# Kernel tuning notes

Measured on AMD Instinct MI355X. Metric: run time of the kernel, lower is better.

Reference implementation:

```python
import jax, jax.numpy as jnp
import numpy as np

MUL = 512
IR_DIMS = (1, 3, 5)          # 0e, 1e, 2e -> 2l+1
PW = MUL ** -0.5             # path_weight = (mul_in * n_paths_to_out)^-0.5, n_paths=1 each


def setup_inputs() -> dict:
    key = jax.random.key(0)
    k_x, k0, k1, k2 = jax.random.split(key, 4)
    B = 4096
    D = MUL * sum(IR_DIMS)  # 4608
    return {
        "x": jax.random.normal(k_x, (B, D), dtype=jnp.float32),
        "w0": jax.random.normal(k0, (MUL, MUL), dtype=jnp.float32),
        "w1": jax.random.normal(k1, (MUL, MUL), dtype=jnp.float32),
        "w2": jax.random.normal(k2, (MUL, MUL), dtype=jnp.float32),
        "b0": jnp.zeros((MUL,), dtype=jnp.float32),  # bias only on scalar 0e irrep
    }


def reference(x, w0, w1, w2, b0):
    B = x.shape[0]
    # split x into per-irrep blocks (B, mul, 2l+1), as Irreps.as_list does
    offs = np.cumsum([0] + [MUL * d for d in IR_DIMS])
    blocks = [x[:, offs[i]:offs[i + 1]].reshape(B, MUL, IR_DIMS[i]) for i in range(3)]
    outs = []
    for blk, w, d in zip(blocks, (w0, w1, w2), IR_DIMS):
        # path_weight * einsum('uw,bui->bwi'), then flatten to mul_ir_out.dim
        o = PW * jnp.einsum('uw,bui->bwi', w, blk)
        outs.append(o.reshape(B, MUL * d))
    # bias instruction: path_weight 1.0, only on the scalar (0e) output irrep
    outs[0] = outs[0] + b0[None, :]
    return jnp.concatenate(outs, axis=-1)
```

## Files before the change

kernel.cpp:

```cpp
#include <hip/hip_runtime.h>


#define BATCH 4096
#define DTOT 4608
#define NMUL 512

typedef __attribute__((ext_vector_type(8))) short short8;
typedef __attribute__((ext_vector_type(8))) unsigned short ushort8;
typedef __attribute__((ext_vector_type(4))) float float4v;

#define XPL_BYTES (9ull * BATCH * NMUL * 2)

__device__ __forceinline__ unsigned short f2bf(float f) {
    unsigned int u = __builtin_bit_cast(unsigned int, f);
    return (unsigned short)((u + 0x7fffu + ((u >> 16) & 1u)) >> 16);
}
__device__ __forceinline__ void gld16(const unsigned short* g, unsigned short* l) {
    __builtin_amdgcn_global_load_lds(
        (const __attribute__((address_space(1))) unsigned int*)(const void*)g,
        (__attribute__((address_space(3))) unsigned int*)(void*)l, 16, 0, 0);
}
__device__ __forceinline__ void colmap(int col, int& c, int& u) {
    if (col < 512)       { c = 0; u = col; }
    else if (col < 2048) { int t = col - 512;  c = 1 + t % 3; u = t / 3; }
    else                 { int t = col - 2048; c = 4 + t % 5; u = t / 5; }
}

__global__ __launch_bounds__(256) void prep(const float* __restrict__ x,
                                            const float* __restrict__ w0,
                                            const float* __restrict__ w1,
                                            const float* __restrict__ w2,
                                            unsigned short* __restrict__ Xp,
                                            unsigned short* __restrict__ Wt) {
    __shared__ unsigned short buf[4608];
    const int tid = threadIdx.x;
    const int b = blockIdx.x;
    if (b < BATCH) {
        const int row = b;
        const float4v* src = (const float4v*)(x + (size_t)row * DTOT);
        for (int p = tid; p < DTOT / 4; p += 256) {
            float4v v = src[p];
#pragma unroll
            for (int j = 0; j < 4; ++j) {
                int c, u; colmap(p * 4 + j, c, u);
                buf[c * NMUL + u] = f2bf(v[j]);
            }
        }
        __syncthreads();
        for (int q = tid; q < DTOT / 8; q += 256) {
            const int c = q >> 6, u8 = q & 63;
            *(ushort8*)(Xp + ((size_t)(c * BATCH + row) * NMUL) + u8 * 8) =
                *(const ushort8*)&buf[c * NMUL + u8 * 8];
        }
    } else {
        const int t = b - BATCH;
        const int ch = t >> 6, tt = t & 63;
        const int tk = (tt >> 3) * 64, tn = (tt & 7) * 64;
        const float* W = (ch == 0) ? w0 : (ch == 1) ? w1 : w2;
        const int r0 = tid >> 4, c4 = (tid & 15) * 4;
#pragma unroll
        for (int rr = 0; rr < 4; ++rr) {
            const int row = r0 + rr * 16;
            float4v v = *(const float4v*)(W + (size_t)(tk + row) * NMUL + tn + c4);
#pragma unroll
            for (int j = 0; j < 4; ++j) buf[(c4 + j) * 72 + row] = f2bf(v[j]);
        }
        __syncthreads();
        for (int q = tid; q < 512; q += 256) {
            const int nn = q >> 3, k8 = q & 7;
            *(ushort8*)(Wt + ((size_t)(ch * NMUL + tn + nn) * NMUL) + tk + k8 * 8) =
                *(const ushort8*)&buf[nn * 72 + k8 * 8];
        }
    }
}

template <int D, int PBASE, int XOFF, int WCH>
__device__ __forceinline__ void body_d35(int rel,
                                         const unsigned short* __restrict__ Xp,
                                         const unsigned short* __restrict__ Wt,
                                         float* __restrict__ out,
                                         unsigned short* As, unsigned short* Bs) {
    float* Cs = (float*)As;

    const int tid = threadIdx.x;
    const int lane = tid & 63;
    const int w = tid >> 6;
    const int lr = lane & 15;
    const int lq = lane >> 4;

    const int n0 = (rel & 7) * 64;
    const int m0 = (rel >> 3) * 64;

    const unsigned short* Ag =
        Xp + ((size_t)(PBASE + w) * BATCH + m0 + (lane >> 2)) * NMUL + (lane & 3) * 8;
    const unsigned short* Bg =
        Wt + ((size_t)WCH * NMUL + n0 + (lane >> 2)) * NMUL + (lane & 3) * 8;
    unsigned short* Al = As + w * 2048;

    float4v acc[4][4];
#pragma unroll
    for (int a = 0; a < 4; ++a)
#pragma unroll
        for (int b = 0; b < 4; ++b) acc[a][b] = (float4v)0.f;

    for (int kt = 0; kt < 16; ++kt) {
        const int ko = kt * 32;
        if (w < D) {
#pragma unroll
            for (int p = 0; p < 4; ++p)
                gld16(Ag + (size_t)p * 16 * NMUL + ko, Al + p * 512);
            for (int p = w; p < 4; p += D)
                gld16(Bg + (size_t)p * 16 * NMUL + ko, Bs + p * 512);
        }
        __syncthreads();
        if (w < D) {
            short8 af[4], bf[4];
#pragma unroll
            for (int mi = 0; mi < 4; ++mi)
                af[mi] = *(const short8*)(Al + (mi * 16 + lr) * 32 + lq * 8);
#pragma unroll
            for (int ni = 0; ni < 4; ++ni)
                bf[ni] = *(const short8*)(Bs + (ni * 16 + lr) * 32 + lq * 8);
#pragma unroll
            for (int mi = 0; mi < 4; ++mi)
#pragma unroll
                for (int ni = 0; ni < 4; ++ni)
                    acc[mi][ni] = __builtin_amdgcn_mfma_f32_16x16x32_bf16(
                        af[mi], bf[ni], acc[mi][ni], 0, 0, 0);
        }
        __syncthreads();
    }

    const float PW = 0.044194173824159216f;
#pragma unroll
    for (int mc = 0; mc < 4; ++mc) {
        if (w < D) {
#pragma unroll
            for (int ni = 0; ni < 4; ++ni)
#pragma unroll
                for (int r = 0; r < 4; ++r)
                    Cs[(lq * 4 + r) * (64 * D) + (ni * 16 + lr) * D + w] =
                        acc[mc][ni][r] * PW;
        }
        __syncthreads();
        constexpr int F4 = 16 * 16 * D;
        for (int f = tid; f < F4; f += 320) {
            const int row = f / (16 * D);
            const int c4  = f % (16 * D);
            *(float4v*)(out + (size_t)(m0 + mc * 16 + row) * DTOT + XOFF + n0 * D + c4 * 4) =
                *(const float4v*)(Cs + f * 4);
        }
        __syncthreads();
    }
}

__device__ __forceinline__ void body_d1(int rel,
                                        const unsigned short* __restrict__ Xp,
                                        const unsigned short* __restrict__ Wt,
                                        const float* __restrict__ b0,
                                        float* __restrict__ out,
                                        unsigned short* As, unsigned short* Bs) {
    const int tid = threadIdx.x;
    const int lane = tid & 63;
    const int w = tid >> 6;
    const int lr = lane & 15;
    const int lq = lane >> 4;
    const int wm = (w >> 1) * 64;
    const int wn = (w & 1) * 64;

    const int n0 = (rel & 3) * 128;
    const int m0 = (rel >> 2) * 128;

    const unsigned short* Ag = Xp + (size_t)(m0 + w * 32 + (lane >> 2)) * NMUL + (lane & 3) * 8;
    const unsigned short* Bg = Wt + (size_t)(n0 + w * 32 + (lane >> 2)) * NMUL + (lane & 3) * 8;
    unsigned short* Al = As + w * 1024;
    unsigned short* Bl = Bs + w * 1024;

    float4v acc[4][4];
#pragma unroll
    for (int a = 0; a < 4; ++a)
#pragma unroll
        for (int b = 0; b < 4; ++b) acc[a][b] = (float4v)0.f;

    for (int kt = 0; kt < 16; ++kt) {
        const int ko = kt * 32;
        if (w < 4) {
            gld16(Ag + ko, Al);
            gld16(Ag + ko + 16 * NMUL, Al + 512);
            gld16(Bg + ko, Bl);
            gld16(Bg + ko + 16 * NMUL, Bl + 512);
        }
        __syncthreads();
        if (w < 4) {
            short8 af[4], bf[4];
#pragma unroll
            for (int mi = 0; mi < 4; ++mi)
                af[mi] = *(const short8*)(As + (wm + mi * 16 + lr) * 32 + lq * 8);
#pragma unroll
            for (int ni = 0; ni < 4; ++ni)
                bf[ni] = *(const short8*)(Bs + (wn + ni * 16 + lr) * 32 + lq * 8);
#pragma unroll
            for (int mi = 0; mi < 4; ++mi)
#pragma unroll
                for (int ni = 0; ni < 4; ++ni)
                    acc[mi][ni] = __builtin_amdgcn_mfma_f32_16x16x32_bf16(
                        af[mi], bf[ni], acc[mi][ni], 0, 0, 0);
        }
        __syncthreads();
    }

    if (w < 4) {
        const float PW = 0.044194173824159216f;
#pragma unroll
        for (int ni = 0; ni < 4; ++ni) {
            const int col = n0 + wn + ni * 16 + lr;
            const float bias = b0[col];
#pragma unroll
            for (int mi = 0; mi < 4; ++mi)
#pragma unroll
                for (int r = 0; r < 4; ++r)
                    out[(size_t)(m0 + wm + mi * 16 + lq * 4 + r) * DTOT + col] =
                        acc[mi][ni][r] * PW + bias;
        }
    }
}

__global__ __launch_bounds__(320) void gemm_all(const unsigned short* __restrict__ Xp,
                                                const unsigned short* __restrict__ Wt,
                                                const float* __restrict__ b0,
                                                float* __restrict__ out) {
    __shared__ __align__(16) unsigned short As[10240];
    __shared__ __align__(16) unsigned short Bs[4096];

    const int b = blockIdx.x;
    if (b < 512)       body_d35<5, 4, 2048, 2>(b, Xp, Wt, out, As, Bs);
    else if (b < 1024) body_d35<3, 1, 512, 1>(b - 512, Xp, Wt, out, As, Bs);
    else               body_d1(b - 1024, Xp, Wt, b0, out, As, Bs);
}

extern "C" void kernel_launch(void* const* d_in, const int* in_sizes, int n_in,
                              void* d_out, int out_size, void* d_ws, size_t ws_size,
                              hipStream_t stream) {
    const float* x  = (const float*)d_in[0];
    const float* w0 = (const float*)d_in[1];
    const float* w1 = (const float*)d_in[2];
    const float* w2 = (const float*)d_in[3];
    const float* b0 = (const float*)d_in[4];
    float* out = (float*)d_out;

    unsigned short* Xp = (unsigned short*)d_ws;
    unsigned short* Wt = (unsigned short*)((char*)d_ws + XPL_BYTES);

    prep<<<dim3(BATCH + 192), dim3(256), 0, stream>>>(x, w0, w1, w2, Xp, Wt);
    gemm_all<<<dim3(1152), dim3(320), 0, stream>>>(Xp, Wt, b0, out);
}
```

Measured before the change: 192.9 us.

## Double-buffer LDS tiles, XOR-swizzle LDS layout, and remap blocks across XCDs

Both GEMM bodies now double-buffer their LDS tiles: the next K-slice is prefetched with global_load_lds while MFMAs run on the current one, which drops one barrier per iteration. Tile columns are XOR-swizzled on load and on read to avoid LDS bank conflicts. Block IDs are remapped so consecutive logical tiles land on the same XCD, improving L2 reuse. LDS use roughly doubles, which can lower occupancy.

```diff
diff --git a/kernel.cpp b/kernel.cpp
--- a/kernel.cpp
+++ b/kernel.cpp
@@ -79,9 +79,8 @@
                                          const unsigned short* __restrict__ Xp,
                                          const unsigned short* __restrict__ Wt,
                                          float* __restrict__ out,
-                                         unsigned short* As, unsigned short* Bs) {
-    float* Cs = (float*)As;
-
+                                         unsigned short (*As)[10240],
+                                         unsigned short (*Bs)[2048]) {
     const int tid = threadIdx.x;
     const int lane = tid & 63;
     const int w = tid >> 6;
@@ -91,11 +90,13 @@
     const int n0 = (rel & 7) * 64;
     const int m0 = (rel >> 3) * 64;
 
+    const int ksw = ((lane & 3) ^ ((lane >> 3) & 3)) * 8;
+    const int rsw = (lq ^ ((lr >> 1) & 3)) * 8;
+
     const unsigned short* Ag =
-        Xp + ((size_t)(PBASE + w) * BATCH + m0 + (lane >> 2)) * NMUL + (lane & 3) * 8;
+        Xp + ((size_t)(PBASE + w) * BATCH + m0 + (lane >> 2)) * NMUL + ksw;
     const unsigned short* Bg =
-        Wt + ((size_t)WCH * NMUL + n0 + (lane >> 2)) * NMUL + (lane & 3) * 8;
-    unsigned short* Al = As + w * 2048;
+        Wt + ((size_t)WCH * NMUL + n0 + (lane >> 2)) * NMUL + ksw;
 
     float4v acc[4][4];
 #pragma unroll
@@ -103,24 +104,37 @@
 #pragma unroll
         for (int b = 0; b < 4; ++b) acc[a][b] = (float4v)0.f;
 
+    if (w < D) {
+#pragma unroll
+        for (int p = 0; p < 4; ++p)
+            gld16(Ag + (size_t)p * 16 * NMUL, As[0] + w * 2048 + p * 512);
+    }
+    if (w < 4) gld16(Bg + (size_t)w * 16 * NMUL, Bs[0] + w * 512);
+    __syncthreads();
+
     for (int kt = 0; kt < 16; ++kt) {
-        const int ko = kt * 32;
+        const int cur = kt & 1;
+        if (kt < 15) {
+            const int ko = (kt + 1) * 32;
+            if (w < D) {
+#pragma unroll
+                for (int p = 0; p < 4; ++p)
+                    gld16(Ag + (size_t)p * 16 * NMUL + ko,
+                          As[cur ^ 1] + w * 2048 + p * 512);
+            }
+            if (w < 4)
+                gld16(Bg + (size_t)w * 16 * NMUL + ko, Bs[cur ^ 1] + w * 512);
+        }
         if (w < D) {
-#pragma unroll
-            for (int p = 0; p < 4; ++p)
-                gld16(Ag + (size_t)p * 16 * NMUL + ko, Al + p * 512);
-            for (int p = w; p < 4; p += D)
-                gld16(Bg + (size_t)p * 16 * NMUL + ko, Bs + p * 512);
-        }
-        __syncthreads();
-        if (w < D) {
+            const unsigned short* Al = As[cur] + w * 2048;
+            const unsigned short* Bl = Bs[cur];
             short8 af[4], bf[4];
 #pragma unroll
             for (int mi = 0; mi < 4; ++mi)
-                af[mi] = *(const short8*)(Al + (mi * 16 + lr) * 32 + lq * 8);
+                af[mi] = *(const short8*)(Al + (mi * 16 + lr) * 32 + rsw);
 #pragma unroll
             for (int ni = 0; ni < 4; ++ni)
-                bf[ni] = *(const short8*)(Bs + (ni * 16 + lr) * 32 + lq * 8);
+                bf[ni] = *(const short8*)(Bl + (ni * 16 + lr) * 32 + rsw);
 #pragma unroll
             for (int mi = 0; mi < 4; ++mi)
 #pragma unroll
@@ -131,6 +145,7 @@
         __syncthreads();
     }
 
+    float* Cs = (float*)As;
     const float PW = 0.044194173824159216f;
 #pragma unroll
     for (int mc = 0; mc < 4; ++mc) {
@@ -159,7 +174,7 @@
                                         const unsigned short* __restrict__ Wt,
                                         const float* __restrict__ b0,
                                         float* __restrict__ out,
-                                        unsigned short* As, unsigned short* Bs) {
+                                        unsigned short (*As)[10240]) {
     const int tid = threadIdx.x;
     const int lane = tid & 63;
     const int w = tid >> 6;
@@ -171,10 +186,11 @@
     const int n0 = (rel & 3) * 128;
     const int m0 = (rel >> 2) * 128;
 
-    const unsigned short* Ag = Xp + (size_t)(m0 + w * 32 + (lane >> 2)) * NMUL + (lane & 3) * 8;
-    const unsigned short* Bg = Wt + (size_t)(n0 + w * 32 + (lane >> 2)) * NMUL + (lane & 3) * 8;
-    unsigned short* Al = As + w * 1024;
-    unsigned short* Bl = Bs + w * 1024;
+    const int ksw = ((lane & 3) ^ ((lane >> 3) & 3)) * 8;
+    const int rsw = (lq ^ ((lr >> 1) & 3)) * 8;
+
+    const unsigned short* Ag = Xp + (size_t)(m0 + w * 32 + (lane >> 2)) * NMUL + ksw;
+    const unsigned short* Bg = Wt + (size_t)(n0 + w * 32 + (lane >> 2)) * NMUL + ksw;
 
     float4v acc[4][4];
 #pragma unroll
@@ -182,23 +198,33 @@
 #pragma unroll
         for (int b = 0; b < 4; ++b) acc[a][b] = (float4v)0.f;
 
+    if (w < 4) {
+        gld16(Ag, As[0] + w * 1024);
+        gld16(Ag + 16 * NMUL, As[0] + w * 1024 + 512);
+        gld16(Bg, As[0] + 4096 + w * 1024);
+        gld16(Bg + 16 * NMUL, As[0] + 4096 + w * 1024 + 512);
+    }
+    __syncthreads();
+
     for (int kt = 0; kt < 16; ++kt) {
-        const int ko = kt * 32;
+        const int cur = kt & 1;
+        if (kt < 15 && w < 4) {
+            const int ko = (kt + 1) * 32;
+            gld16(Ag + ko, As[cur ^ 1] + w * 1024);
+            gld16(Ag + ko + 16 * NMUL, As[cur ^ 1] + w * 1024 + 512);
+            gld16(Bg + ko, As[cur ^ 1] + 4096 + w * 1024);
+            gld16(Bg + ko + 16 * NMUL, As[cur ^ 1] + 4096 + w * 1024 + 512);
+        }
         if (w < 4) {
-            gld16(Ag + ko, Al);
-            gld16(Ag + ko + 16 * NMUL, Al + 512);
-            gld16(Bg + ko, Bl);
-            gld16(Bg + ko + 16 * NMUL, Bl + 512);
-        }
-        __syncthreads();
-        if (w < 4) {
+            const unsigned short* Ab = As[cur];
+            const unsigned short* Bb = As[cur] + 4096;
             short8 af[4], bf[4];
 #pragma unroll
             for (int mi = 0; mi < 4; ++mi)
-                af[mi] = *(const short8*)(As + (wm + mi * 16 + lr) * 32 + lq * 8);
+                af[mi] = *(const short8*)(Ab + (wm + mi * 16 + lr) * 32 + rsw);
 #pragma unroll
             for (int ni = 0; ni < 4; ++ni)
-                bf[ni] = *(const short8*)(Bs + (wn + ni * 16 + lr) * 32 + lq * 8);
+                bf[ni] = *(const short8*)(Bb + (wn + ni * 16 + lr) * 32 + rsw);
 #pragma unroll
             for (int mi = 0; mi < 4; ++mi)
 #pragma unroll
@@ -229,13 +255,16 @@
                                                 const unsigned short* __restrict__ Wt,
                                                 const float* __restrict__ b0,
                                                 float* __restrict__ out) {
-    __shared__ __align__(16) unsigned short As[10240];
-    __shared__ __align__(16) unsigned short Bs[4096];
-
-    const int b = blockIdx.x;
+    __shared__ __align__(16) unsigned short As[2][10240];
+    __shared__ __align__(16) unsigned short Bs[2][2048];
+
+    const int hw = blockIdx.x;
+    const int xcd = hw & 7, j = hw >> 3;
+    const int b = ((xcd + ((j >> 3) << 3)) << 3) + (j & 7);
+
     if (b < 512)       body_d35<5, 4, 2048, 2>(b, Xp, Wt, out, As, Bs);
     else if (b < 1024) body_d35<3, 1, 512, 1>(b - 512, Xp, Wt, out, As, Bs);
-    else               body_d1(b - 1024, Xp, Wt, b0, out, As, Bs);
+    else               body_d1(b - 1024, Xp, Wt, b0, out, As);
 }
 
 extern "C" void kernel_launch(void* const* d_in, const int* in_sizes, int n_in,
```

Result: faster. 177.3 us (-8.1%).

## Swizzle LDS tiles, remap blocks across XCDs, and lighten GEMM barriers

Applied to the files above, without the earlier changes.

Applies an XOR swizzle to the k-chunk offsets in both the global-to-LDS loads and the LDS fragment reads to reduce bank conflicts. Remaps block indices so neighbouring output tiles land on the same XCD for better L2 reuse of shared A/B panels. Replaces __syncthreads with explicit vmcnt/lgkmcnt waits plus s_barrier, and raises wave priority around the MFMA loop. The LDS footprint also shrinks: the B tile is spread across the first four waves and body_d1 packs its B tile into As. The swizzle must stay consistent between writers and readers, and the XCD remap assumes the grid is a multiple of 64 blocks.

```diff
diff --git a/kernel.cpp b/kernel.cpp
--- a/kernel.cpp
+++ b/kernel.cpp
@@ -19,6 +19,12 @@
     __builtin_amdgcn_global_load_lds(
         (const __attribute__((address_space(1))) unsigned int*)(const void*)g,
         (__attribute__((address_space(3))) unsigned int*)(void*)l, 16, 0, 0);
+}
+__device__ __forceinline__ void waitvm0() {
+    asm volatile("s_waitcnt vmcnt(0)" ::: "memory");
+}
+__device__ __forceinline__ void waitlgkm0() {
+    asm volatile("s_waitcnt lgkmcnt(0)" ::: "memory");
 }
 __device__ __forceinline__ void colmap(int col, int& c, int& u) {
     if (col < 512)       { c = 0; u = col; }
@@ -79,9 +85,8 @@
                                          const unsigned short* __restrict__ Xp,
                                          const unsigned short* __restrict__ Wt,
                                          float* __restrict__ out,
-                                         unsigned short* As, unsigned short* Bs) {
-    float* Cs = (float*)As;
-
+                                         unsigned short* As,
+                                         unsigned short* Bs) {
     const int tid = threadIdx.x;
     const int lane = tid & 63;
     const int w = tid >> 6;
@@ -91,10 +96,13 @@
     const int n0 = (rel & 7) * 64;
     const int m0 = (rel >> 3) * 64;
 
+    const int ksw = ((lane & 3) ^ ((lane >> 3) & 3)) * 8;
+    const int rsw = (lq ^ ((lr >> 1) & 3)) * 8;
+
     const unsigned short* Ag =
-        Xp + ((size_t)(PBASE + w) * BATCH + m0 + (lane >> 2)) * NMUL + (lane & 3) * 8;
+        Xp + ((size_t)(PBASE + w) * BATCH + m0 + (lane >> 2)) * NMUL + ksw;
     const unsigned short* Bg =
-        Wt + ((size_t)WCH * NMUL + n0 + (lane >> 2)) * NMUL + (lane & 3) * 8;
+        Wt + ((size_t)WCH * NMUL + n0 + (lane >> 2)) * NMUL + ksw;
     unsigned short* Al = As + w * 2048;
 
     float4v acc[4][4];
@@ -109,28 +117,34 @@
 #pragma unroll
             for (int p = 0; p < 4; ++p)
                 gld16(Ag + (size_t)p * 16 * NMUL + ko, Al + p * 512);
-            for (int p = w; p < 4; p += D)
-                gld16(Bg + (size_t)p * 16 * NMUL + ko, Bs + p * 512);
-        }
-        __syncthreads();
+        }
+        if (w < 4)
+            gld16(Bg + (size_t)w * 16 * NMUL + ko, Bs + w * 512);
+        waitvm0();
+        __builtin_amdgcn_s_barrier();
         if (w < D) {
+            const unsigned short* Bl = Bs;
             short8 af[4], bf[4];
 #pragma unroll
             for (int mi = 0; mi < 4; ++mi)
-                af[mi] = *(const short8*)(Al + (mi * 16 + lr) * 32 + lq * 8);
+                af[mi] = *(const short8*)(Al + (mi * 16 + lr) * 32 + rsw);
 #pragma unroll
             for (int ni = 0; ni < 4; ++ni)
-                bf[ni] = *(const short8*)(Bs + (ni * 16 + lr) * 32 + lq * 8);
+                bf[ni] = *(const short8*)(Bl + (ni * 16 + lr) * 32 + rsw);
+            __builtin_amdgcn_s_setprio(1);
 #pragma unroll
             for (int mi = 0; mi < 4; ++mi)
 #pragma unroll
                 for (int ni = 0; ni < 4; ++ni)
                     acc[mi][ni] = __builtin_amdgcn_mfma_f32_16x16x32_bf16(
                         af[mi], bf[ni], acc[mi][ni], 0, 0, 0);
-        }
-        __syncthreads();
-    }
-
+            __builtin_amdgcn_s_setprio(0);
+        }
+        waitlgkm0();
+        __builtin_amdgcn_s_barrier();
+    }
+
+    float* Cs = (float*)As;
     const float PW = 0.044194173824159216f;
 #pragma unroll
     for (int mc = 0; mc < 4; ++mc) {
@@ -159,7 +173,7 @@
                                         const unsigned short* __restrict__ Wt,
                                         const float* __restrict__ b0,
                                         float* __restrict__ out,
-                                        unsigned short* As, unsigned short* Bs) {
+                                        unsigned short* As) {
     const int tid = threadIdx.x;
     const int lane = tid & 63;
     const int w = tid >> 6;
@@ -171,10 +185,13 @@
     const int n0 = (rel & 3) * 128;
     const int m0 = (rel >> 2) * 128;
 
-    const unsigned short* Ag = Xp + (size_t)(m0 + w * 32 + (lane >> 2)) * NMUL + (lane & 3) * 8;
-    const unsigned short* Bg = Wt + (size_t)(n0 + w * 32 + (lane >> 2)) * NMUL + (lane & 3) * 8;
+    const int ksw = ((lane & 3) ^ ((lane >> 3) & 3)) * 8;
+    const int rsw = (lq ^ ((lr >> 1) & 3)) * 8;
+
+    const unsigned short* Ag = Xp + (size_t)(m0 + w * 32 + (lane >> 2)) * NMUL + ksw;
+    const unsigned short* Bg = Wt + (size_t)(n0 + w * 32 + (lane >> 2)) * NMUL + ksw;
     unsigned short* Al = As + w * 1024;
-    unsigned short* Bl = Bs + w * 1024;
+    unsigned short* Bl = As + 4096 + w * 1024;
 
     float4v acc[4][4];
 #pragma unroll
@@ -190,23 +207,29 @@
             gld16(Bg + ko, Bl);
             gld16(Bg + ko + 16 * NMUL, Bl + 512);
         }
-        __syncthreads();
+        waitvm0();
+        __builtin_amdgcn_s_barrier();
         if (w < 4) {
+            const unsigned short* Ab = As;
+            const unsigned short* Bb = As + 4096;
             short8 af[4], bf[4];
 #pragma unroll
             for (int mi = 0; mi < 4; ++mi)
-                af[mi] = *(const short8*)(As + (wm + mi * 16 + lr) * 32 + lq * 8);
+                af[mi] = *(const short8*)(Ab + (wm + mi * 16 + lr) * 32 + rsw);
 #pragma unroll
             for (int ni = 0; ni < 4; ++ni)
-                bf[ni] = *(const short8*)(Bs + (wn + ni * 16 + lr) * 32 + lq * 8);
+                bf[ni] = *(const short8*)(Bb + (wn + ni * 16 + lr) * 32 + rsw);
+            __builtin_amdgcn_s_setprio(1);
 #pragma unroll
             for (int mi = 0; mi < 4; ++mi)
 #pragma unroll
                 for (int ni = 0; ni < 4; ++ni)
                     acc[mi][ni] = __builtin_amdgcn_mfma_f32_16x16x32_bf16(
                         af[mi], bf[ni], acc[mi][ni], 0, 0, 0);
-        }
-        __syncthreads();
+            __builtin_amdgcn_s_setprio(0);
+        }
+        waitlgkm0();
+        __builtin_amdgcn_s_barrier();
     }
 
     if (w < 4) {
@@ -230,12 +253,15 @@
                                                 const float* __restrict__ b0,
                                                 float* __restrict__ out) {
     __shared__ __align__(16) unsigned short As[10240];
-    __shared__ __align__(16) unsigned short Bs[4096];
-
-    const int b = blockIdx.x;
+    __shared__ __align__(16) unsigned short Bs[2048];
+
+    const int hw = blockIdx.x;
+    const int xcd = hw & 7, j = hw >> 3;
+    const int b = ((xcd + ((j >> 3) << 3)) << 3) + (j & 7);
+
     if (b < 512)       body_d35<5, 4, 2048, 2>(b, Xp, Wt, out, As, Bs);
     else if (b < 1024) body_d35<3, 1, 512, 1>(b - 512, Xp, Wt, out, As, Bs);
-    else               body_d1(b - 1024, Xp, Wt, b0, out, As, Bs);
+    else               body_d1(b - 1024, Xp, Wt, b0, out, As);
 }
 
 extern "C" void kernel_launch(void* const* d_in, const int* in_sizes, int n_in,
```

Measured after the change: 180.2 us. 1.07x faster.

## Load MFMA operands directly from global, drop LDS staging, remap blocks to XCDs

Applied to the files above, without the earlier changes.

The GEMM main loops no longer stage A/B tiles through LDS with global_load_lds and two barriers per k-step. Each wave now loads its MFMA fragments straight from global memory into registers, with unroll 2 and s_setprio raised around the MFMA burst. The block index is also permuted so that groups of 8 consecutive logical tiles land on the same XCD, which should improve L2 reuse of shared X/W rows. The cost is redundant global traffic, since waves sharing B (or A in body_d1) each fetch it separately, and the fragment loads are 16-byte strided rows that lean on the L2 cache.

```diff
diff --git a/kernel.cpp b/kernel.cpp
--- a/kernel.cpp
+++ b/kernel.cpp
@@ -14,11 +14,6 @@
 __device__ __forceinline__ unsigned short f2bf(float f) {
     unsigned int u = __builtin_bit_cast(unsigned int, f);
     return (unsigned short)((u + 0x7fffu + ((u >> 16) & 1u)) >> 16);
-}
-__device__ __forceinline__ void gld16(const unsigned short* g, unsigned short* l) {
-    __builtin_amdgcn_global_load_lds(
-        (const __attribute__((address_space(1))) unsigned int*)(const void*)g,
-        (__attribute__((address_space(3))) unsigned int*)(void*)l, 16, 0, 0);
 }
 __device__ __forceinline__ void colmap(int col, int& c, int& u) {
     if (col < 512)       { c = 0; u = col; }
@@ -79,9 +74,7 @@
                                          const unsigned short* __restrict__ Xp,
                                          const unsigned short* __restrict__ Wt,
                                          float* __restrict__ out,
-                                         unsigned short* As, unsigned short* Bs) {
-    float* Cs = (float*)As;
-
+                                         unsigned short* As) {
     const int tid = threadIdx.x;
     const int lane = tid & 63;
     const int w = tid >> 6;
@@ -91,46 +84,39 @@
     const int n0 = (rel & 7) * 64;
     const int m0 = (rel >> 3) * 64;
 
-    const unsigned short* Ag =
-        Xp + ((size_t)(PBASE + w) * BATCH + m0 + (lane >> 2)) * NMUL + (lane & 3) * 8;
-    const unsigned short* Bg =
-        Wt + ((size_t)WCH * NMUL + n0 + (lane >> 2)) * NMUL + (lane & 3) * 8;
-    unsigned short* Al = As + w * 2048;
-
     float4v acc[4][4];
 #pragma unroll
     for (int a = 0; a < 4; ++a)
 #pragma unroll
         for (int b = 0; b < 4; ++b) acc[a][b] = (float4v)0.f;
 
-    for (int kt = 0; kt < 16; ++kt) {
-        const int ko = kt * 32;
-        if (w < D) {
-#pragma unroll
-            for (int p = 0; p < 4; ++p)
-                gld16(Ag + (size_t)p * 16 * NMUL + ko, Al + p * 512);
-            for (int p = w; p < 4; p += D)
-                gld16(Bg + (size_t)p * 16 * NMUL + ko, Bs + p * 512);
-        }
-        __syncthreads();
-        if (w < D) {
+    if (w < D) {
+        const unsigned short* Ab =
+            Xp + ((size_t)(PBASE + w) * BATCH + m0 + lr) * NMUL + lq * 8;
+        const unsigned short* Bb =
+            Wt + ((size_t)WCH * NMUL + n0 + lr) * NMUL + lq * 8;
+#pragma unroll 2
+        for (int kt = 0; kt < 16; ++kt) {
+            const int ko = kt * 32;
             short8 af[4], bf[4];
 #pragma unroll
             for (int mi = 0; mi < 4; ++mi)
-                af[mi] = *(const short8*)(Al + (mi * 16 + lr) * 32 + lq * 8);
+                af[mi] = *(const short8*)(Ab + (size_t)mi * 16 * NMUL + ko);
 #pragma unroll
             for (int ni = 0; ni < 4; ++ni)
-                bf[ni] = *(const short8*)(Bs + (ni * 16 + lr) * 32 + lq * 8);
+                bf[ni] = *(const short8*)(Bb + (size_t)ni * 16 * NMUL + ko);
+            __builtin_amdgcn_s_setprio(1);
 #pragma unroll
             for (int mi = 0; mi < 4; ++mi)
 #pragma unroll
                 for (int ni = 0; ni < 4; ++ni)
                     acc[mi][ni] = __builtin_amdgcn_mfma_f32_16x16x32_bf16(
                         af[mi], bf[ni], acc[mi][ni], 0, 0, 0);
-        }
-        __syncthreads();
-    }
-
+            __builtin_amdgcn_s_setprio(0);
+        }
+    }
+
+    float* Cs = (float*)As;
     const float PW = 0.044194173824159216f;
 #pragma unroll
     for (int mc = 0; mc < 4; ++mc) {
@@ -158,11 +144,11 @@
                                         const unsigned short* __restrict__ Xp,
                                         const unsigned short* __restrict__ Wt,
                                         const float* __restrict__ b0,
-                                        float* __restrict__ out,
-                                        unsigned short* As, unsigned short* Bs) {
+                                        float* __restrict__ out) {
     const int tid = threadIdx.x;
     const int lane = tid & 63;
     const int w = tid >> 6;
+    if (w >= 4) return;
     const int lr = lane & 15;
     const int lq = lane >> 4;
     const int wm = (w >> 1) * 64;
@@ -171,10 +157,8 @@
     const int n0 = (rel & 3) * 128;
     const int m0 = (rel >> 2) * 128;
 
-    const unsigned short* Ag = Xp + (size_t)(m0 + w * 32 + (lane >> 2)) * NMUL + (lane & 3) * 8;
-    const unsigned short* Bg = Wt + (size_t)(n0 + w * 32 + (lane >> 2)) * NMUL + (lane & 3) * 8;
-    unsigned short* Al = As + w * 1024;
-    unsigned short* Bl = Bs + w * 1024;
+    const unsigned short* Ab = Xp + (size_t)(m0 + wm + lr) * NMUL + lq * 8;
+    const unsigned short* Bb = Wt + (size_t)(n0 + wn + lr) * NMUL + lq * 8;
 
     float4v acc[4][4];
 #pragma unroll
@@ -182,46 +166,37 @@
 #pragma unroll
         for (int b = 0; b < 4; ++b) acc[a][b] = (float4v)0.f;
 
+#pragma unroll 2
     for (int kt = 0; kt < 16; ++kt) {
         const int ko = kt * 32;
-        if (w < 4) {
-            gld16(Ag + ko, Al);
-            gld16(Ag + ko + 16 * NMUL, Al + 512);
-            gld16(Bg + ko, Bl);
-            gld16(Bg + ko + 16 * NMUL, Bl + 512);
-        }
-        __syncthreads();
-        if (w < 4) {
-            short8 af[4], bf[4];
-#pragma unroll
-            for (int mi = 0; mi < 4; ++mi)
-                af[mi] = *(const short8*)(As + (wm + mi * 16 + lr) * 32 + lq * 8);
+        short8 af[4], bf[4];
+#pragma unroll
+        for (int mi = 0; mi < 4; ++mi)
+            af[mi] = *(const short8*)(Ab + (size_t)mi * 16 * NMUL + ko);
+#pragma unroll
+        for (int ni = 0; ni < 4; ++ni)
+            bf[ni] = *(const short8*)(Bb + (size_t)ni * 16 * NMUL + ko);
+        __builtin_amdgcn_s_setprio(1);
+#pragma unroll
+        for (int mi = 0; mi < 4; ++mi)
 #pragma unroll
             for (int ni = 0; ni < 4; ++ni)
-                bf[ni] = *(const short8*)(Bs + (wn + ni * 16 + lr) * 32 + lq * 8);
-#pragma unroll
-            for (int mi = 0; mi < 4; ++mi)
-#pragma unroll
-                for (int ni = 0; ni < 4; ++ni)
-                    acc[mi][ni] = __builtin_amdgcn_mfma_f32_16x16x32_bf16(
-                        af[mi], bf[ni], acc[mi][ni], 0, 0, 0);
-        }
-        __syncthreads();
-    }
-
-    if (w < 4) {
-        const float PW = 0.044194173824159216f;
-#pragma unroll
-        for (int ni = 0; ni < 4; ++ni) {
-            const int col = n0 + wn + ni * 16 + lr;
-            const float bias = b0[col];
-#pragma unroll
-            for (int mi = 0; mi < 4; ++mi)
-#pragma unroll
-                for (int r = 0; r < 4; ++r)
-                    out[(size_t)(m0 + wm + mi * 16 + lq * 4 + r) * DTOT + col] =
-                        acc[mi][ni][r] * PW + bias;
-        }
+                acc[mi][ni] = __builtin_amdgcn_mfma_f32_16x16x32_bf16(
+                    af[mi], bf[ni], acc[mi][ni], 0, 0, 0);
+        __builtin_amdgcn_s_setprio(0);
+    }
+
+    const float PW = 0.044194173824159216f;
+#pragma unroll
+    for (int ni = 0; ni < 4; ++ni) {
+        const int col = n0 + wn + ni * 16 + lr;
+        const float bias = b0[col];
+#pragma unroll
+        for (int mi = 0; mi < 4; ++mi)
+#pragma unroll
+            for (int r = 0; r < 4; ++r)
+                out[(size_t)(m0 + wm + mi * 16 + lq * 4 + r) * DTOT + col] =
+                    acc[mi][ni][r] * PW + bias;
     }
 }
 
@@ -230,12 +205,14 @@
                                                 const float* __restrict__ b0,
                                                 float* __restrict__ out) {
     __shared__ __align__(16) unsigned short As[10240];
-    __shared__ __align__(16) unsigned short Bs[4096];
-
-    const int b = blockIdx.x;
-    if (b < 512)       body_d35<5, 4, 2048, 2>(b, Xp, Wt, out, As, Bs);
-    else if (b < 1024) body_d35<3, 1, 512, 1>(b - 512, Xp, Wt, out, As, Bs);
-    else               body_d1(b - 1024, Xp, Wt, b0, out, As, Bs);
+
+    const int hw = blockIdx.x;
+    const int xcd = hw & 7, j = hw >> 3;
+    const int b = ((xcd + ((j >> 3) << 3)) << 3) + (j & 7);
+
+    if (b < 512)       body_d35<5, 4, 2048, 2>(b, Xp, Wt, out, As);
+    else if (b < 1024) body_d35<3, 1, 512, 1>(b - 512, Xp, Wt, out, As);
+    else               body_d1(b - 1024, Xp, Wt, b0, out);
 }
 
 extern "C" void kernel_launch(void* const* d_in, const int* in_sizes, int n_in,
```

Result: slower. 217.5 us (+12.7%).
